# Kernel optimization log

Measured on AMD Instinct MI355X. Metric: run time of the kernel, lower is better.

The kernel has to match this reference:

```python
import jax, jax.numpy as jnp
import numpy as np

B, T, C, H = 8, 2048, 1024, 64  # batch, seq (== block_size), n_embd, head_size


def setup_inputs() -> dict:
    key = jax.random.key(0)
    k1, k2, k3, k4 = jax.random.split(key, 4)
    x = jax.random.normal(k1, (B, T, C), dtype=jnp.float32)
    scale = 0.02
    Wk = jax.random.normal(k2, (H, C), dtype=jnp.float32) * scale  # nn.Linear weight [out,in]
    Wq = jax.random.normal(k3, (H, C), dtype=jnp.float32) * scale
    Wv = jax.random.normal(k4, (H, C), dtype=jnp.float32) * scale
    return {"x": x, "Wk": Wk, "Wq": Wq, "Wv": Wv}


def reference(x, Wk, Wq, Wv):
    # k, q, v projections (bias-free linears): x @ W.T
    k = jnp.einsum('btc,hc->bth', x, Wk)
    q = jnp.einsum('btc,hc->bth', x, Wq)
    v = jnp.einsum('btc,hc->bth', x, Wv)
    # NOTE: source MULTIPLIES by sqrt(head_size) (faithful to original code)
    wei = jnp.einsum('bth,bsh->bts', q, k) * (H ** 0.5)  # [B,T,T]
    causal = jnp.tril(jnp.ones((T, T), dtype=bool))
    wei = jnp.where(causal, wei, -jnp.inf)
    wei = jax.nn.softmax(wei, axis=-1)
    # dropout_value = 0.0 -> identity (deterministic baseline)
    out = jnp.einsum('bts,bsh->bth', wei, v)  # [B,T,H]
    return out
```

## Files before the change

### kernel.cpp

```cpp
#include <hip/hip_runtime.h>

#define BB 8
#define TT 2048
#define CC 1024
#define HH 64
#define MM (BB * TT)

typedef _Float16 half8 __attribute__((ext_vector_type(8)));
typedef float floatx4 __attribute__((ext_vector_type(4)));

__global__ __launch_bounds__(256)
void w_convert(const float* __restrict__ Wk, const float* __restrict__ Wq,
               const float* __restrict__ Wv, _Float16* __restrict__ W16)
{
    const int e = (blockIdx.x * 256 + threadIdx.x) * 8;
    const int row = e >> 10;
    const int c   = e & 1023;
    const int which = row >> 6;
    const float* __restrict__ src = (which == 0) ? Wq : ((which == 1) ? Wk : Wv);
    const float scale = (which == 0) ? 8.0f : 1.0f;
    const int srow = row & 63;
    const float4 a = *reinterpret_cast<const float4*>(&src[srow * 1024 + c]);
    const float4 b = *reinterpret_cast<const float4*>(&src[srow * 1024 + c + 4]);
    const half8 o = { (_Float16)(a.x * scale), (_Float16)(a.y * scale),
                      (_Float16)(a.z * scale), (_Float16)(a.w * scale),
                      (_Float16)(b.x * scale), (_Float16)(b.y * scale),
                      (_Float16)(b.z * scale), (_Float16)(b.w * scale) };
    *reinterpret_cast<half8*>(&W16[e]) = o;
}

__global__ __launch_bounds__(256, 2)
void qkv_fused(const float* __restrict__ x, const _Float16* __restrict__ W16,
               _Float16* __restrict__ q16, _Float16* __restrict__ k16,
               _Float16* __restrict__ v16)
{
    __shared__ _Float16 Xs[64 * 72];
    __shared__ _Float16 Ws[192 * 72];

    const int m_base = blockIdx.x * 64;
    const int tid  = threadIdx.x;
    const int lane = tid & 63;
    const int wv   = tid >> 6;
    const int fm   = lane & 15;
    const int fk   = (lane >> 4) * 8;
    const int fr   = (lane >> 4) * 4;

    const int srow = tid >> 2;
    const int sk   = (tid & 3) * 16;

    floatx4 acc[4][3];
    #pragma unroll
    for (int m = 0; m < 4; ++m)
        #pragma unroll
        for (int n = 0; n < 3; ++n)
            #pragma unroll
            for (int r = 0; r < 4; ++r) acc[m][n][r] = 0.0f;

    float4 xr[4];
    half8  wr[6];

    {
        const float* xp = &x[(size_t)(m_base + srow) * CC + sk];
        #pragma unroll
        for (int i = 0; i < 4; ++i) xr[i] = *reinterpret_cast<const float4*>(xp + i * 4);
        #pragma unroll
        for (int i = 0; i < 6; ++i) {
            const int cch = tid + i * 256;
            const int wrow = cch >> 3, wk = (cch & 7) * 8;
            wr[i] = *reinterpret_cast<const half8*>(&W16[(size_t)wrow * CC + wk]);
        }
    }

    for (int c = 0; c < 16; ++c) {
        __syncthreads();
        #pragma unroll
        for (int p = 0; p < 2; ++p) {
            const float4 a = xr[p * 2], b = xr[p * 2 + 1];
            const half8 h = { (_Float16)a.x, (_Float16)a.y, (_Float16)a.z, (_Float16)a.w,
                              (_Float16)b.x, (_Float16)b.y, (_Float16)b.z, (_Float16)b.w };
            *reinterpret_cast<half8*>(&Xs[srow * 72 + sk + p * 8]) = h;
        }
        #pragma unroll
        for (int i = 0; i < 6; ++i) {
            const int cch = tid + i * 256;
            const int wrow = cch >> 3, wk = (cch & 7) * 8;
            *reinterpret_cast<half8*>(&Ws[wrow * 72 + wk]) = wr[i];
        }
        __syncthreads();

        if (c < 15) {
            const int k0 = (c + 1) * 64;
            const float* xp = &x[(size_t)(m_base + srow) * CC + k0 + sk];
            #pragma unroll
            for (int i = 0; i < 4; ++i) xr[i] = *reinterpret_cast<const float4*>(xp + i * 4);
            #pragma unroll
            for (int i = 0; i < 6; ++i) {
                const int cch = tid + i * 256;
                const int wrow = cch >> 3, wk = (cch & 7) * 8;
                wr[i] = *reinterpret_cast<const half8*>(&W16[(size_t)wrow * CC + k0 + wk]);
            }
        }

        #pragma unroll
        for (int kc = 0; kc < 2; ++kc) {
            half8 af[4];
            #pragma unroll
            for (int m = 0; m < 4; ++m)
                af[m] = *reinterpret_cast<const half8*>(&Xs[(m * 16 + fm) * 72 + kc * 32 + fk]);
            #pragma unroll
            for (int n = 0; n < 3; ++n) {
                const half8 bf = *reinterpret_cast<const half8*>(
                    &Ws[((wv * 3 + n) * 16 + fm) * 72 + kc * 32 + fk]);
                #pragma unroll
                for (int m = 0; m < 4; ++m)
                    acc[m][n] = __builtin_amdgcn_mfma_f32_16x16x32_f16(af[m], bf, acc[m][n], 0, 0, 0);
            }
        }
    }

    #pragma unroll
    for (int n = 0; n < 3; ++n) {
        const int col = (wv * 3 + n) * 16 + fm;
        const int which = col >> 6;
        const int h = col & 63;
        _Float16* __restrict__ outp = (which == 0) ? q16 : ((which == 1) ? k16 : v16);
        #pragma unroll
        for (int m = 0; m < 4; ++m)
            #pragma unroll
            for (int r = 0; r < 4; ++r)
                outp[(size_t)(m_base + m * 16 + fr + r) * HH + h] = (_Float16)acc[m][n][r];
    }
}

__global__ __launch_bounds__(256, 4)
void v_transpose(const _Float16* __restrict__ v16, _Float16* __restrict__ vt16)
{
    __shared__ _Float16 Ts[64 * 72];
    const int bid = blockIdx.x;
    const int b = bid >> 5, tile = bid & 31;
    const int tid = threadIdx.x;

    #pragma unroll
    for (int i = 0; i < 2; ++i) {
        const int s = i * 256 + tid;
        const int row = s >> 3, cq = (s & 7) * 8;
        *reinterpret_cast<half8*>(&Ts[row * 72 + cq]) =
            *reinterpret_cast<const half8*>(&v16[((size_t)b * TT + tile * 64 + row) * HH + cq]);
    }
    __syncthreads();
    #pragma unroll
    for (int i = 0; i < 2; ++i) {
        const int s = i * 256 + tid;
        const int h = s >> 3, tq = (s & 7) * 8;
        half8 o;
        #pragma unroll
        for (int jj = 0; jj < 8; ++jj) o[jj] = Ts[(tq + jj) * 72 + h];
        *reinterpret_cast<half8*>(&vt16[((size_t)b * HH + h) * TT + tile * 64 + tq]) = o;
    }
}

__global__ __launch_bounds__(128, 4)
void attn(const _Float16* __restrict__ q16, const _Float16* __restrict__ k16,
          const _Float16* __restrict__ vt16, float* __restrict__ out)
{
    __shared__ _Float16 Ks[64 * 72];
    __shared__ _Float16 Vts[64 * 72];
    __shared__ _Float16 Ps[2 * 16 * 72];

    const int bid = blockIdx.x;
    const int b  = bid & 7;
    const int it = 63 - (bid >> 3);
    const int tid  = threadIdx.x;
    const int lane = tid & 63;
    const int wv   = tid >> 6;
    const int fm   = lane & 15;
    const int fk   = (lane >> 4) * 8;
    const int fr   = (lane >> 4) * 4;

    const _Float16* __restrict__ qb  = q16  + (size_t)b * TT * HH;
    const _Float16* __restrict__ kb  = k16  + (size_t)b * TT * HH;
    const _Float16* __restrict__ vtb = vt16 + (size_t)b * HH * TT;

    const int qrow = it * 32 + wv * 16 + fm;
    const half8 qf0 = *reinterpret_cast<const half8*>(&qb[(size_t)qrow * HH + fk]);
    const half8 qf1 = *reinterpret_cast<const half8*>(&qb[(size_t)qrow * HH + 32 + fk]);

    floatx4 O[4];
    float m_r[4], l_r[4];
    #pragma unroll
    for (int r = 0; r < 4; ++r) {
        m_r[r] = -3.0e38f; l_r[r] = 0.0f;
        #pragma unroll
        for (int ht = 0; ht < 4; ++ht) O[ht][r] = 0.0f;
    }

    const int Ji = (it >> 1) + 1;
    const int sr = tid >> 3;
    const int sc = (tid & 7) * 8;

    half8 kr[4], vr[4];
    #pragma unroll
    for (int i = 0; i < 4; ++i) {
        kr[i] = *reinterpret_cast<const half8*>(&kb[(size_t)(sr + i * 16) * HH + sc]);
        vr[i] = *reinterpret_cast<const half8*>(&vtb[(size_t)(sr + i * 16) * TT + sc]);
    }

    for (int j = 0; j < Ji; ++j) {
        __syncthreads();
        #pragma unroll
        for (int i = 0; i < 4; ++i) {
            *reinterpret_cast<half8*>(&Ks[(sr + i * 16) * 72 + sc])  = kr[i];
            *reinterpret_cast<half8*>(&Vts[(sr + i * 16) * 72 + sc]) = vr[i];
        }
        __syncthreads();

        if (j + 1 < Ji) {
            const int jn = (j + 1) * 64;
            #pragma unroll
            for (int i = 0; i < 4; ++i) {
                kr[i] = *reinterpret_cast<const half8*>(&kb[(size_t)(jn + sr + i * 16) * HH + sc]);
                vr[i] = *reinterpret_cast<const half8*>(&vtb[(size_t)(sr + i * 16) * TT + jn + sc]);
            }
        }

        floatx4 sa[4];
        #pragma unroll
        for (int nt = 0; nt < 4; ++nt) {
            #pragma unroll
            for (int r = 0; r < 4; ++r) sa[nt][r] = 0.0f;
            const _Float16* kp = &Ks[(nt * 16 + fm) * 72];
            const half8 b0 = *reinterpret_cast<const half8*>(kp + fk);
            const half8 b1 = *reinterpret_cast<const half8*>(kp + 32 + fk);
            sa[nt] = __builtin_amdgcn_mfma_f32_16x16x32_f16(qf0, b0, sa[nt], 0, 0, 0);
            sa[nt] = __builtin_amdgcn_mfma_f32_16x16x32_f16(qf1, b1, sa[nt], 0, 0, 0);
        }

        if (j == Ji - 1) {
            const int rbase = it * 32 + wv * 16 + fr;
            #pragma unroll
            for (int nt = 0; nt < 4; ++nt) {
                const int col = j * 64 + nt * 16 + fm;
                #pragma unroll
                for (int r = 0; r < 4; ++r)
                    if (col > rbase + r) sa[nt][r] = -3.0e38f;
            }
        }

        #pragma unroll
        for (int r = 0; r < 4; ++r) {
            float mx = fmaxf(fmaxf(sa[0][r], sa[1][r]), fmaxf(sa[2][r], sa[3][r]));
            #pragma unroll
            for (int off = 1; off < 16; off <<= 1)
                mx = fmaxf(mx, __shfl_xor(mx, off, 16));
            const float mn = fmaxf(m_r[r], mx);
            const float alpha = __expf(m_r[r] - mn);
            const float p0 = __expf(sa[0][r] - mn);
            const float p1 = __expf(sa[1][r] - mn);
            const float p2 = __expf(sa[2][r] - mn);
            const float p3 = __expf(sa[3][r] - mn);
            _Float16* pp = &Ps[wv * 1152 + (fr + r) * 72 + fm];
            pp[0]  = (_Float16)p0;
            pp[16] = (_Float16)p1;
            pp[32] = (_Float16)p2;
            pp[48] = (_Float16)p3;
            float sum = p0 + p1 + p2 + p3;
            #pragma unroll
            for (int off = 1; off < 16; off <<= 1)
                sum += __shfl_xor(sum, off, 16);
            l_r[r] = l_r[r] * alpha + sum;
            m_r[r] = mn;
            O[0][r] *= alpha; O[1][r] *= alpha; O[2][r] *= alpha; O[3][r] *= alpha;
        }
        __syncthreads();

        #pragma unroll
        for (int ch = 0; ch < 2; ++ch) {
            const half8 pa = *reinterpret_cast<const half8*>(
                &Ps[wv * 1152 + fm * 72 + ch * 32 + fk]);
            #pragma unroll
            for (int ht = 0; ht < 4; ++ht) {
                const half8 vb = *reinterpret_cast<const half8*>(
                    &Vts[(ht * 16 + fm) * 72 + ch * 32 + fk]);
                O[ht] = __builtin_amdgcn_mfma_f32_16x16x32_f16(pa, vb, O[ht], 0, 0, 0);
            }
        }
    }

    #pragma unroll
    for (int r = 0; r < 4; ++r) {
        const float inv = 1.0f / l_r[r];
        const size_t rowoff = (size_t)(b * TT + it * 32 + wv * 16 + fr + r) * HH;
        #pragma unroll
        for (int ht = 0; ht < 4; ++ht)
            out[rowoff + ht * 16 + fm] = O[ht][r] * inv;
    }
}

extern "C" void kernel_launch(void* const* d_in, const int* in_sizes, int n_in,
                              void* d_out, int out_size, void* d_ws, size_t ws_size,
                              hipStream_t stream)
{
    (void)in_sizes; (void)n_in; (void)out_size; (void)ws_size;

    const float* x  = (const float*)d_in[0];
    const float* Wk = (const float*)d_in[1];
    const float* Wq = (const float*)d_in[2];
    const float* Wv = (const float*)d_in[3];
    float* out = (float*)d_out;

    _Float16* q16  = (_Float16*)d_ws;
    _Float16* k16  = q16 + (size_t)MM * HH;
    _Float16* v16  = k16 + (size_t)MM * HH;
    _Float16* vt16 = v16 + (size_t)MM * HH;
    _Float16* W16  = vt16 + (size_t)MM * HH;

    w_convert<<<dim3(96), dim3(256), 0, stream>>>(Wk, Wq, Wv, W16);
    qkv_fused<<<dim3(256), dim3(256), 0, stream>>>(x, W16, q16, k16, v16);
    v_transpose<<<dim3(256), dim3(256), 0, stream>>>(v16, vt16);
    attn<<<dim3(512), dim3(128), 0, stream>>>(q16, k16, vt16, out);
}
```

Measured before the change: 177.3 us.

## Rewrite QKV projection without LDS, fuse V transpose, use MFMA row-sum and DPP max

Replaces the LDS-tiled QKV GEMM with a per-wave direct-from-global MFMA kernel that double-buffers register loads and writes V already transposed, removing the separate transpose kernel and its launch. In attention, the row max reduction uses DPP instead of shuffles, and the softmax denominator is accumulated with an extra MFMA against a ones vector instead of shuffle sums. Occupancy hint drops to 3 and the block order interleaves long and short causal tiles. Risks: direct global loads without LDS reuse W repeatedly, raising memory traffic, and the fp16-rounded P now feeds the denominator.

Result: slower. 182.4 us (+2.9%).

```diff
diff --git a/kernel.cpp b/kernel.cpp
--- a/kernel.cpp
+++ b/kernel.cpp
@@ -7,7 +7,25 @@
 #define MM (BB * TT)
 
 typedef _Float16 half8 __attribute__((ext_vector_type(8)));
+typedef _Float16 half4 __attribute__((ext_vector_type(4)));
 typedef float floatx4 __attribute__((ext_vector_type(4)));
+
+template <int CTRL>
+__device__ __forceinline__ float dpp_max_step(float x)
+{
+    union { float f; int i; } u, v;
+    u.f = x;
+    v.i = __builtin_amdgcn_update_dpp(u.i, u.i, CTRL, 0xf, 0xf, false);
+    return fmaxf(x, v.f);
+}
+__device__ __forceinline__ float rowmax16(float x)
+{
+    x = dpp_max_step<0x128>(x);
+    x = dpp_max_step<0x124>(x);
+    x = dpp_max_step<0x122>(x);
+    x = dpp_max_step<0x121>(x);
+    return x;
+}
 
 __global__ __launch_bounds__(256)
 void w_convert(const float* __restrict__ Wk, const float* __restrict__ Wq,
@@ -29,15 +47,104 @@
     *reinterpret_cast<half8*>(&W16[e]) = o;
 }
 
-__global__ __launch_bounds__(256, 2)
-void qkv_fused(const float* __restrict__ x, const _Float16* __restrict__ W16,
-               _Float16* __restrict__ q16, _Float16* __restrict__ k16,
-               _Float16* __restrict__ v16)
-{
-    __shared__ _Float16 Xs[64 * 72];
-    __shared__ _Float16 Ws[192 * 72];
-
-    const int m_base = blockIdx.x * 64;
+__device__ __forceinline__ void qkv_loadA(const float* __restrict__ xrow, int k0,
+                                          float4& xa, float4& xb)
+{
+    xa = *reinterpret_cast<const float4*>(xrow + k0);
+    xb = *reinterpret_cast<const float4*>(xrow + k0 + 4);
+}
+__device__ __forceinline__ void qkv_loadB(const _Float16* __restrict__ wbase, int k0,
+                                          half8 (&bf)[12])
+{
+    #pragma unroll
+    for (int n = 0; n < 12; ++n)
+        bf[n] = *reinterpret_cast<const half8*>(wbase + (size_t)n * 16 * CC + k0);
+}
+__device__ __forceinline__ void qkv_mfma(const float4& xa, const float4& xb,
+                                         const half8 (&bf)[12], floatx4 (&acc)[12])
+{
+    const half8 af = { (_Float16)xa.x, (_Float16)xa.y, (_Float16)xa.z, (_Float16)xa.w,
+                       (_Float16)xb.x, (_Float16)xb.y, (_Float16)xb.z, (_Float16)xb.w };
+    #pragma unroll
+    for (int n = 0; n < 12; ++n)
+        acc[n] = __builtin_amdgcn_mfma_f32_16x16x32_f16(af, bf[n], acc[n], 0, 0, 0);
+}
+
+__global__ __launch_bounds__(256, 1)
+void qkv_direct(const float* __restrict__ x, const _Float16* __restrict__ W16,
+                _Float16* __restrict__ q16, _Float16* __restrict__ k16,
+                _Float16* __restrict__ vt16)
+{
+    const int tid  = threadIdx.x;
+    const int lane = tid & 63;
+    const int wv   = tid >> 6;
+    const int tile = blockIdx.x * 4 + wv;
+    const int m_base = tile * 16;
+    const int fm = lane & 15;
+    const int fq = lane >> 4;
+    const int fk = fq * 8;
+    const int fr = fq * 4;
+
+    const float*     __restrict__ xrow  = &x[(size_t)(m_base + fm) * CC + fk];
+    const _Float16*  __restrict__ wbase = &W16[(size_t)fm * CC + fk];
+
+    floatx4 acc[12];
+    #pragma unroll
+    for (int n = 0; n < 12; ++n)
+        #pragma unroll
+        for (int r = 0; r < 4; ++r) acc[n][r] = 0.0f;
+
+    float4 xa0, xb0, xa1, xb1;
+    half8 bf0[12], bf1[12];
+
+    qkv_loadA(xrow, 0, xa0, xb0);
+    qkv_loadB(wbase, 0, bf0);
+
+    #pragma unroll 2
+    for (int c = 0; c < 32; c += 2) {
+        qkv_loadA(xrow, (c + 1) * 32, xa1, xb1);
+        qkv_loadB(wbase, (c + 1) * 32, bf1);
+        qkv_mfma(xa0, xb0, bf0, acc);
+        if (c + 2 < 32) {
+            qkv_loadA(xrow, (c + 2) * 32, xa0, xb0);
+            qkv_loadB(wbase, (c + 2) * 32, bf0);
+        }
+        qkv_mfma(xa1, xb1, bf1, acc);
+    }
+
+    const int b  = m_base >> 11;
+    const int t0 = m_base & 2047;
+    #pragma unroll
+    for (int n = 0; n < 12; ++n) {
+        const int col = n * 16 + fm;
+        if (n < 8) {
+            _Float16* __restrict__ dst = (n < 4) ? q16 : k16;
+            const int h = col & 63;
+            #pragma unroll
+            for (int r = 0; r < 4; ++r)
+                dst[(size_t)(m_base + fr + r) * HH + h] = (_Float16)acc[n][r];
+        } else {
+            const int h = col - 128;
+            const half4 pk = { (_Float16)acc[n][0], (_Float16)acc[n][1],
+                               (_Float16)acc[n][2], (_Float16)acc[n][3] };
+            *reinterpret_cast<half4*>(
+                &vt16[((size_t)b * HH + h) * TT + t0 + fr]) = pk;
+        }
+    }
+}
+
+__global__ __launch_bounds__(128, 3)
+void attn(const _Float16* __restrict__ q16, const _Float16* __restrict__ k16,
+          const _Float16* __restrict__ vt16, float* __restrict__ out)
+{
+    __shared__ _Float16 Ks[64 * 72];
+    __shared__ _Float16 Vts[64 * 72];
+    __shared__ _Float16 Ps[2 * 16 * 72];
+
+    const int bid = blockIdx.x;
+    const int b = bid & 7;
+    const int g = bid >> 3;
+    const int it = (g < 32) ? (63 - g) : (g - 32);
     const int tid  = threadIdx.x;
     const int lane = tid & 63;
     const int wv   = tid >> 6;
@@ -45,138 +152,6 @@
     const int fk   = (lane >> 4) * 8;
     const int fr   = (lane >> 4) * 4;
 
-    const int srow = tid >> 2;
-    const int sk   = (tid & 3) * 16;
-
-    floatx4 acc[4][3];
-    #pragma unroll
-    for (int m = 0; m < 4; ++m)
-        #pragma unroll
-        for (int n = 0; n < 3; ++n)
-            #pragma unroll
-            for (int r = 0; r < 4; ++r) acc[m][n][r] = 0.0f;
-
-    float4 xr[4];
-    half8  wr[6];
-
-    {
-        const float* xp = &x[(size_t)(m_base + srow) * CC + sk];
-        #pragma unroll
-        for (int i = 0; i < 4; ++i) xr[i] = *reinterpret_cast<const float4*>(xp + i * 4);
-        #pragma unroll
-        for (int i = 0; i < 6; ++i) {
-            const int cch = tid + i * 256;
-            const int wrow = cch >> 3, wk = (cch & 7) * 8;
-            wr[i] = *reinterpret_cast<const half8*>(&W16[(size_t)wrow * CC + wk]);
-        }
-    }
-
-    for (int c = 0; c < 16; ++c) {
-        __syncthreads();
-        #pragma unroll
-        for (int p = 0; p < 2; ++p) {
-            const float4 a = xr[p * 2], b = xr[p * 2 + 1];
-            const half8 h = { (_Float16)a.x, (_Float16)a.y, (_Float16)a.z, (_Float16)a.w,
-                              (_Float16)b.x, (_Float16)b.y, (_Float16)b.z, (_Float16)b.w };
-            *reinterpret_cast<half8*>(&Xs[srow * 72 + sk + p * 8]) = h;
-        }
-        #pragma unroll
-        for (int i = 0; i < 6; ++i) {
-            const int cch = tid + i * 256;
-            const int wrow = cch >> 3, wk = (cch & 7) * 8;
-            *reinterpret_cast<half8*>(&Ws[wrow * 72 + wk]) = wr[i];
-        }
-        __syncthreads();
-
-        if (c < 15) {
-            const int k0 = (c + 1) * 64;
-            const float* xp = &x[(size_t)(m_base + srow) * CC + k0 + sk];
-            #pragma unroll
-            for (int i = 0; i < 4; ++i) xr[i] = *reinterpret_cast<const float4*>(xp + i * 4);
-            #pragma unroll
-            for (int i = 0; i < 6; ++i) {
-                const int cch = tid + i * 256;
-                const int wrow = cch >> 3, wk = (cch & 7) * 8;
-                wr[i] = *reinterpret_cast<const half8*>(&W16[(size_t)wrow * CC + k0 + wk]);
-            }
-        }
-
-        #pragma unroll
-        for (int kc = 0; kc < 2; ++kc) {
-            half8 af[4];
-            #pragma unroll
-            for (int m = 0; m < 4; ++m)
-                af[m] = *reinterpret_cast<const half8*>(&Xs[(m * 16 + fm) * 72 + kc * 32 + fk]);
-            #pragma unroll
-            for (int n = 0; n < 3; ++n) {
-                const half8 bf = *reinterpret_cast<const half8*>(
-                    &Ws[((wv * 3 + n) * 16 + fm) * 72 + kc * 32 + fk]);
-                #pragma unroll
-                for (int m = 0; m < 4; ++m)
-                    acc[m][n] = __builtin_amdgcn_mfma_f32_16x16x32_f16(af[m], bf, acc[m][n], 0, 0, 0);
-            }
-        }
-    }
-
-    #pragma unroll
-    for (int n = 0; n < 3; ++n) {
-        const int col = (wv * 3 + n) * 16 + fm;
-        const int which = col >> 6;
-        const int h = col & 63;
-        _Float16* __restrict__ outp = (which == 0) ? q16 : ((which == 1) ? k16 : v16);
-        #pragma unroll
-        for (int m = 0; m < 4; ++m)
-            #pragma unroll
-            for (int r = 0; r < 4; ++r)
-                outp[(size_t)(m_base + m * 16 + fr + r) * HH + h] = (_Float16)acc[m][n][r];
-    }
-}
-
-__global__ __launch_bounds__(256, 4)
-void v_transpose(const _Float16* __restrict__ v16, _Float16* __restrict__ vt16)
-{
-    __shared__ _Float16 Ts[64 * 72];
-    const int bid = blockIdx.x;
-    const int b = bid >> 5, tile = bid & 31;
-    const int tid = threadIdx.x;
-
-    #pragma unroll
-    for (int i = 0; i < 2; ++i) {
-        const int s = i * 256 + tid;
-        const int row = s >> 3, cq = (s & 7) * 8;
-        *reinterpret_cast<half8*>(&Ts[row * 72 + cq]) =
-            *reinterpret_cast<const half8*>(&v16[((size_t)b * TT + tile * 64 + row) * HH + cq]);
-    }
-    __syncthreads();
-    #pragma unroll
-    for (int i = 0; i < 2; ++i) {
-        const int s = i * 256 + tid;
-        const int h = s >> 3, tq = (s & 7) * 8;
-        half8 o;
-        #pragma unroll
-        for (int jj = 0; jj < 8; ++jj) o[jj] = Ts[(tq + jj) * 72 + h];
-        *reinterpret_cast<half8*>(&vt16[((size_t)b * HH + h) * TT + tile * 64 + tq]) = o;
-    }
-}
-
-__global__ __launch_bounds__(128, 4)
-void attn(const _Float16* __restrict__ q16, const _Float16* __restrict__ k16,
-          const _Float16* __restrict__ vt16, float* __restrict__ out)
-{
-    __shared__ _Float16 Ks[64 * 72];
-    __shared__ _Float16 Vts[64 * 72];
-    __shared__ _Float16 Ps[2 * 16 * 72];
-
-    const int bid = blockIdx.x;
-    const int b  = bid & 7;
-    const int it = 63 - (bid >> 3);
-    const int tid  = threadIdx.x;
-    const int lane = tid & 63;
-    const int wv   = tid >> 6;
-    const int fm   = lane & 15;
-    const int fk   = (lane >> 4) * 8;
-    const int fr   = (lane >> 4) * 4;
-
     const _Float16* __restrict__ qb  = q16  + (size_t)b * TT * HH;
     const _Float16* __restrict__ kb  = k16  + (size_t)b * TT * HH;
     const _Float16* __restrict__ vtb = vt16 + (size_t)b * HH * TT;
@@ -185,14 +160,18 @@
     const half8 qf0 = *reinterpret_cast<const half8*>(&qb[(size_t)qrow * HH + fk]);
     const half8 qf1 = *reinterpret_cast<const half8*>(&qb[(size_t)qrow * HH + 32 + fk]);
 
-    floatx4 O[4];
-    float m_r[4], l_r[4];
+    floatx4 O[4], lacc;
+    float m_r[4];
     #pragma unroll
     for (int r = 0; r < 4; ++r) {
-        m_r[r] = -3.0e38f; l_r[r] = 0.0f;
+        m_r[r] = -3.0e38f;
+        lacc[r] = 0.0f;
         #pragma unroll
         for (int ht = 0; ht < 4; ++ht) O[ht][r] = 0.0f;
     }
+
+    const half8 ones = { (_Float16)1.f, (_Float16)1.f, (_Float16)1.f, (_Float16)1.f,
+                         (_Float16)1.f, (_Float16)1.f, (_Float16)1.f, (_Float16)1.f };
 
     const int Ji = (it >> 1) + 1;
     const int sr = tid >> 3;
@@ -249,26 +228,16 @@
         #pragma unroll
         for (int r = 0; r < 4; ++r) {
             float mx = fmaxf(fmaxf(sa[0][r], sa[1][r]), fmaxf(sa[2][r], sa[3][r]));
-            #pragma unroll
-            for (int off = 1; off < 16; off <<= 1)
-                mx = fmaxf(mx, __shfl_xor(mx, off, 16));
+            mx = rowmax16(mx);
             const float mn = fmaxf(m_r[r], mx);
             const float alpha = __expf(m_r[r] - mn);
-            const float p0 = __expf(sa[0][r] - mn);
-            const float p1 = __expf(sa[1][r] - mn);
-            const float p2 = __expf(sa[2][r] - mn);
-            const float p3 = __expf(sa[3][r] - mn);
+            m_r[r] = mn;
             _Float16* pp = &Ps[wv * 1152 + (fr + r) * 72 + fm];
-            pp[0]  = (_Float16)p0;
-            pp[16] = (_Float16)p1;
-            pp[32] = (_Float16)p2;
-            pp[48] = (_Float16)p3;
-            float sum = p0 + p1 + p2 + p3;
-            #pragma unroll
-            for (int off = 1; off < 16; off <<= 1)
-                sum += __shfl_xor(sum, off, 16);
-            l_r[r] = l_r[r] * alpha + sum;
-            m_r[r] = mn;
+            pp[0]  = (_Float16)__expf(sa[0][r] - mn);
+            pp[16] = (_Float16)__expf(sa[1][r] - mn);
+            pp[32] = (_Float16)__expf(sa[2][r] - mn);
+            pp[48] = (_Float16)__expf(sa[3][r] - mn);
+            lacc[r] *= alpha;
             O[0][r] *= alpha; O[1][r] *= alpha; O[2][r] *= alpha; O[3][r] *= alpha;
         }
         __syncthreads();
@@ -277,6 +246,7 @@
         for (int ch = 0; ch < 2; ++ch) {
             const half8 pa = *reinterpret_cast<const half8*>(
                 &Ps[wv * 1152 + fm * 72 + ch * 32 + fk]);
+            lacc = __builtin_amdgcn_mfma_f32_16x16x32_f16(pa, ones, lacc, 0, 0, 0);
             #pragma unroll
             for (int ht = 0; ht < 4; ++ht) {
                 const half8 vb = *reinterpret_cast<const half8*>(
@@ -288,7 +258,7 @@
 
     #pragma unroll
     for (int r = 0; r < 4; ++r) {
-        const float inv = 1.0f / l_r[r];
+        const float inv = 1.0f / lacc[r];
         const size_t rowoff = (size_t)(b * TT + it * 32 + wv * 16 + fr + r) * HH;
         #pragma unroll
         for (int ht = 0; ht < 4; ++ht)
@@ -310,12 +280,10 @@
 
     _Float16* q16  = (_Float16*)d_ws;
     _Float16* k16  = q16 + (size_t)MM * HH;
-    _Float16* v16  = k16 + (size_t)MM * HH;
-    _Float16* vt16 = v16 + (size_t)MM * HH;
+    _Float16* vt16 = k16 + (size_t)MM * HH;
     _Float16* W16  = vt16 + (size_t)MM * HH;
 
     w_convert<<<dim3(96), dim3(256), 0, stream>>>(Wk, Wq, Wv, W16);
-    qkv_fused<<<dim3(256), dim3(256), 0, stream>>>(x, W16, q16, k16, v16);
-    v_transpose<<<dim3(256), dim3(256), 0, stream>>>(v16, vt16);
+    qkv_direct<<<dim3(256), dim3(256), 0, stream>>>(x, W16, q16, k16, vt16);
     attn<<<dim3(512), dim3(128), 0, stream>>>(q16, k16, vt16, out);
 }
```
